# Optimization experiments

Hardware: AMD Instinct MI355X
Metric: run time of the kernel (lower is better)

The kernel has to match this reference:

```python
import jax, jax.numpy as jnp
import numpy as np

B, N, D, K = 8, 2048, 512, 16  # batch, points, feature dim, similar_num
EPS = 1e-8


def setup_inputs() -> dict:
    key = jax.random.key(0)
    ks = jax.random.split(key, 9)
    p = jax.random.normal(ks[0], (B, N, 3), dtype=jnp.float32)
    q = jax.random.normal(ks[1], (B, N, 3), dtype=jnp.float32)
    ffp = jax.random.normal(ks[2], (B, N, D), dtype=jnp.float32)
    ffq = jax.random.normal(ks[3], (B, N, D), dtype=jnp.float32)
    eye = jnp.eye(3, dtype=jnp.float32)
    # near-identity perturbed rotations so inverse is well-conditioned
    R1 = eye + 0.1 * jax.random.normal(ks[4], (B, N, 3, 3), dtype=jnp.float32)
    R2 = eye + 0.1 * jax.random.normal(ks[5], (B, N, 3, 3), dtype=jnp.float32)
    centroids = jax.random.randint(ks[6], (B, N), 0, 2 * N)  # FPS indices into 2N pts
    W = 0.02 * jax.random.normal(ks[7], (3, 3 * D), dtype=jnp.float32)  # refine_net pointwise linear
    b = jnp.zeros((3,), dtype=jnp.float32)
    return {"p": p, "q": q, "ffp": ffp, "ffq": ffq, "R1": R1, "R2": R2,
            "centroids": centroids, "W": W, "b": b}


def _forward(p, q, ffp, ffq, R1, R2, centroids, W, b):
    # cosine similarity between query features (ffq) and source features (ffp): [B,N,N]
    fq = ffq / (jnp.linalg.norm(ffq, axis=-1, keepdims=True) + EPS)
    fp = ffp / (jnp.linalg.norm(ffp, axis=-1, keepdims=True) + EPS)
    w1 = jnp.einsum('bqd,bpd->bqp', fq, fp)
    _, idx = jax.lax.top_k(w1, K)                      # [B,N,K] neighbor indices into ffp
    feat = jax.vmap(lambda z, i: z[i])(ffp, idx)       # batched gather -> [B,N,K,D]
    # adaptive_{avg,max}_pool2d over the K axis, then cat(avg, max): [B,N,2D]
    f_agg = jnp.concatenate([feat.mean(axis=2), feat.max(axis=2)], axis=-1)
    f1 = jnp.concatenate([ffq, f_agg], axis=-1)        # [B,N,3D]
    vec = jnp.einsum('bnd,od->bno', f1, W) + b         # refine_net -> [B,N,3]
    vec = jnp.linalg.inv(R1) @ vec[..., None]          # rotate back (R1^-1)
    vec = (jnp.linalg.inv(R2) @ vec)[..., 0]           # rotate back (R2^-1) -> [B,N,3]
    mask = (centroids >= p.shape[1]).astype(vec.dtype)[..., None]
    q_refine = q + vec * mask
    return q_refine, idx


def reference(p, q, ffp, ffq, R1, R2, centroids, W, b):
    q_refine, similar_idx = _forward(p, q, ffp, ffq, R1, R2, centroids, W, b)
    # original returns (q_cat, q_refine, q_refine, similar_idx)
    return (q, q_refine, q_refine, similar_idx)
```

## Files before the change

kernel.cpp:

```cpp
#include <hip/hip_runtime.h>
#include <math.h>

#define BB 8
#define NN 2048
#define DD 512
#define KK 16
#define BN (BB*NN)

#define QT 64
#define JSPLIT 4
#define JRANGE (NN/JSPLIT)
#define MM (16*JSPLIT)
#define SIMP 68

#define KSPLIT 384

#define OUT1 (BN*3)
#define OUT2 (2*BN*3)
#define OUT3 (3*BN*3)

typedef __attribute__((ext_vector_type(8))) short bf16x8;
typedef __attribute__((ext_vector_type(4))) float f32x4;

__device__ inline unsigned short cvt_bf16(float f) {
    unsigned int u = __float_as_uint(f);
    return (unsigned short)((u + 0x7fffu + ((u >> 16) & 1u)) >> 16);
}

__device__ inline void gload_lds16(const unsigned short* g, unsigned short* lds) {
    __builtin_amdgcn_global_load_lds((const __attribute__((address_space(1))) void*)g,
                                     (__attribute__((address_space(3))) void*)lds,
                                     16, 0, 0);
}

__global__ __launch_bounds__(256) void k_norm_np(const float* __restrict__ ffq,
                                                 const float* __restrict__ ffp,
                                                 float* __restrict__ normq,
                                                 float* __restrict__ normp,
                                                 float* __restrict__ rnp32) {
    const int row = blockIdx.x * 32 + (threadIdx.x >> 3);
    const int j   = threadIdx.x & 7;
    const bool isQ = row < BN;
    const int r = isQ ? row : row - BN;
    const float* x = (isQ ? ffq : ffp) + (size_t)r * DD;

    float B[4];
#pragma unroll
    for (int t = 0; t < 4; ++t) {
        const float* xb = x + t * 128;
        float e = xb[j];
        float rj = __fmul_rn(e, e);
#pragma unroll
        for (int i = 1; i < 16; ++i) {
            float v = xb[8 * i + j];
            rj = __fadd_rn(rj, __fmul_rn(v, v));
        }
        float s = __fadd_rn(rj, __shfl_xor(rj, 1, 8));
        float u = __fadd_rn(s,  __shfl_xor(s,  2, 8));
        float w = __fadd_rn(u,  __shfl_xor(u,  4, 8));
        B[t] = w;
    }
    if (j == 0) {
        float norm2 = __fadd_rn(__fadd_rn(B[0], B[1]), __fadd_rn(B[2], B[3]));
        float nrm = __fsqrt_rn(norm2);
        if (isQ) { normq[r] = nrm; }
        else {
            normp[r] = nrm;
            rnp32[r] = 1.0f / __fadd_rn(nrm, 1e-8f);
        }
    }
}

__global__ __launch_bounds__(256) void k_normalize(const float* __restrict__ ffq,
                                                   const float* __restrict__ ffp,
                                                   const float* __restrict__ normq,
                                                   const float* __restrict__ normp,
                                                   float* __restrict__ fqn,
                                                   float* __restrict__ fpn,
                                                   unsigned short* __restrict__ fqb,
                                                   unsigned short* __restrict__ fpb) {
    const size_t e4 = ((size_t)blockIdx.x * 256 + threadIdx.x) * 4;
    if (e4 >= (size_t)BN * DD) return;
    const int row = (int)(e4 >> 9);
    {
        float4 v = *(const float4*)(ffq + e4);
        float den = __fadd_rn(normq[row], 1e-8f);
        float4 o;
        o.x = __fdiv_rn(v.x, den); o.y = __fdiv_rn(v.y, den);
        o.z = __fdiv_rn(v.z, den); o.w = __fdiv_rn(v.w, den);
        *(float4*)(fqn + e4) = o;
        ushort4 b; b.x = cvt_bf16(o.x); b.y = cvt_bf16(o.y);
        b.z = cvt_bf16(o.z); b.w = cvt_bf16(o.w);
        *(ushort4*)(fqb + e4) = b;
    }
    {
        float4 v = *(const float4*)(ffp + e4);
        float den = __fadd_rn(normp[row], 1e-8f);
        float4 o;
        o.x = __fdiv_rn(v.x, den); o.y = __fdiv_rn(v.y, den);
        o.z = __fdiv_rn(v.z, den); o.w = __fdiv_rn(v.w, den);
        *(float4*)(fpn + e4) = o;
        ushort4 b; b.x = cvt_bf16(o.x); b.y = cvt_bf16(o.y);
        b.z = cvt_bf16(o.z); b.w = cvt_bf16(o.w);
        *(ushort4*)(fpb + e4) = b;
    }
}

#define CK 128
__global__ __launch_bounds__(256, 4) void k_phase1_m(const unsigned short* __restrict__ fqb,
                                                     const unsigned short* __restrict__ fpb,
                                                     unsigned short* __restrict__ cand) {
    __shared__ __align__(16) float simb[QT * SIMP];
    __shared__ __align__(16) unsigned short Bst[64 * CK];

    const int b  = blockIdx.x & 7;
    const int i0 = ((blockIdx.x >> 3) & 31) * QT;
    const int js = blockIdx.x >> 8;
    const int tid = threadIdx.x;
    const int w = tid >> 6, lane = tid & 63;
    const int n16 = lane & 15, quad = lane >> 4;

    const unsigned short* Aq = fqb + ((size_t)b * NN + i0 + w * 16 + n16) * DD + quad * 8;

    float tv[16]; int tix[16];
#pragma unroll
    for (int r = 0; r < 16; ++r) { tv[r] = -INFINITY; tix[r] = -1; }

    const int qq = tid >> 2;
    const int st = tid & 3;
    const size_t bNN = (size_t)b * NN;

    for (int jt = 0; jt < JRANGE / 64; ++jt) {
        const int j0g = js * JRANGE + jt * 64;

        f32x4 acc[4];
#pragma unroll
        for (int ct = 0; ct < 4; ++ct) acc[ct] = (f32x4){0.f, 0.f, 0.f, 0.f};

        for (int kc = 0; kc < 4; ++kc) {
            __syncthreads();
#pragma unroll
            for (int l = 0; l < 4; ++l) {
                const int r  = (w * 4 + l) * 4 + quad;
                const int sb = n16 ^ (r & 15);
                const unsigned short* gsrc =
                    fpb + (bNN + j0g + r) * DD + kc * CK + sb * 8;
                gload_lds16(gsrc, &Bst[(w * 4 + l) * 512]);
            }
            int koff = kc * 128;
            asm volatile("" : "+v"(koff));
            bf16x8 a0 = *(const bf16x8*)(Aq + koff);
            bf16x8 a1 = *(const bf16x8*)(Aq + koff + 32);
            bf16x8 a2 = *(const bf16x8*)(Aq + koff + 64);
            bf16x8 a3 = *(const bf16x8*)(Aq + koff + 96);
            __syncthreads();
#pragma unroll
            for (int k4 = 0; k4 < 4; ++k4) {
                const bf16x8 af = (k4 == 0) ? a0 : (k4 == 1) ? a1 : (k4 == 2) ? a2 : a3;
#pragma unroll
                for (int ct = 0; ct < 4; ++ct) {
                    const int r  = ct * 16 + n16;
                    const int cb = (k4 * 4 + quad) ^ (r & 15);
                    bf16x8 bfr = *(const bf16x8*)&Bst[r * CK + cb * 8];
                    acc[ct] = __builtin_amdgcn_mfma_f32_16x16x32_bf16(
                        af, bfr, acc[ct], 0, 0, 0);
                }
            }
        }

        __syncthreads();
#pragma unroll
        for (int ct = 0; ct < 4; ++ct)
#pragma unroll
            for (int r = 0; r < 4; ++r)
                simb[(w * 16 + quad * 4 + r) * SIMP + ct * 16 + n16] = acc[ct][r];
        __syncthreads();

#pragma unroll
        for (int t4 = 0; t4 < 4; ++t4) {
            const float4 v4 = *(const float4*)&simb[qq * SIMP + st * 16 + t4 * 4];
            const float vm = fmaxf(fmaxf(v4.x, v4.y), fmaxf(v4.z, v4.w));
            if (vm > tv[0]) {
                const float vv[4] = {v4.x, v4.y, v4.z, v4.w};
#pragma unroll
                for (int u = 0; u < 4; ++u) {
                    const float v = vv[u];
                    const int jg = j0g + st * 16 + t4 * 4 + u;
                    if (v > tv[0]) {
#pragma unroll
                        for (int r = 0; r < 15; ++r) {
                            const bool up = tv[r + 1] < v;
                            const float nv = up ? tv[r + 1] : ((tv[r] < v) ? v : tv[r]);
                            const int   ni = up ? tix[r + 1] : ((tv[r] < v) ? jg : tix[r]);
                            tv[r] = nv; tix[r] = ni;
                        }
                        if (tv[15] < v) { tv[15] = v; tix[15] = jg; }
                    }
                }
            }
        }
    }

    __syncthreads();
    int p = 15;
    const size_t base = ((size_t)b * NN + i0 + qq) * MM + (size_t)js * 16;
    for (int m = 0; m < 16; ++m) {
        float cv = (p >= 0) ? tv[p] : -INFINITY;
        int   ci = (p >= 0) ? tix[p] : -1;
        float ov; int oi;
        ov = __shfl_xor(cv, 1, 4); oi = __shfl_xor(ci, 1, 4);
        if (ov > cv || (ov == cv && (unsigned)oi < (unsigned)ci)) { cv = ov; ci = oi; }
        ov = __shfl_xor(cv, 2, 4); oi = __shfl_xor(ci, 2, 4);
        if (ov > cv || (ov == cv && (unsigned)oi < (unsigned)ci)) { cv = ov; ci = oi; }
        if (p >= 0 && tv[p] == cv && tix[p] == ci) --p;
        if (st == 0) cand[base + m] = (unsigned short)ci;
    }
}

#define JTILE 64
#define BK 16
#define LDP 68
__global__ __launch_bounds__(256, 4) void k_phase1_v(const float* __restrict__ ffq,
                                                     const float* __restrict__ ffp,
                                                     const float* __restrict__ rnp32,
                                                     unsigned short* __restrict__ cand) {
    __shared__ __align__(16) float As[BK * LDP];
    __shared__ __align__(16) float Bs[BK * LDP];
    __shared__ __align__(16) float simb[QT * SIMP];

    const int b  = blockIdx.x & 7;
    const int i0 = ((blockIdx.x >> 3) & 31) * QT;
    const int js = blockIdx.x >> 8;
    const int tid = threadIdx.x;
    const int tx = tid & 15, ty = tid >> 4;

    const float* Abase = ffq + ((size_t)b * NN + i0) * DD;
    const float* Bbase = ffp + (size_t)b * NN * DD;

    float tv[16]; int tix[16];
#pragma unroll
    for (int r = 0; r < 16; ++r) { tv[r] = -INFINITY; tix[r] = -1; }

    const int lrow = tid >> 2;
    const int lseg = (tid & 3) * 4;
    const int qq = tid >> 2;
    const int st = tid & 3;

    for (int jt = 0; jt < JRANGE / JTILE; ++jt) {
        const int j0 = js * JRANGE + jt * JTILE;
        float acc[4][4];
#pragma unroll
        for (int r = 0; r < 4; ++r)
#pragma unroll
            for (int c = 0; c < 4; ++c) acc[r][c] = 0.0f;

        for (int kt = 0; kt < DD / BK; ++kt) {
            const int k0 = kt * BK;
            __syncthreads();
            float4 av = *(const float4*)(Abase + (size_t)lrow * DD + k0 + lseg);
            float4 bv = *(const float4*)(Bbase + (size_t)(j0 + lrow) * DD + k0 + lseg);
            As[(lseg + 0) * LDP + lrow] = av.x; As[(lseg + 1) * LDP + lrow] = av.y;
            As[(lseg + 2) * LDP + lrow] = av.z; As[(lseg + 3) * LDP + lrow] = av.w;
            Bs[(lseg + 0) * LDP + lrow] = bv.x; Bs[(lseg + 1) * LDP + lrow] = bv.y;
            Bs[(lseg + 2) * LDP + lrow] = bv.z; Bs[(lseg + 3) * LDP + lrow] = bv.w;
            __syncthreads();
#pragma unroll
            for (int kk = 0; kk < BK; ++kk) {
                const float4 a4 = *(const float4*)&As[kk * LDP + ty * 4];
                const float4 b4 = *(const float4*)&Bs[kk * LDP + tx * 4];
                const float ar[4] = {a4.x, a4.y, a4.z, a4.w};
                const float br[4] = {b4.x, b4.y, b4.z, b4.w};
#pragma unroll
                for (int r = 0; r < 4; ++r)
#pragma unroll
                    for (int c = 0; c < 4; ++c)
                        acc[r][c] = fmaf(ar[r], br[c], acc[r][c]);
            }
        }
        float rp[4];
#pragma unroll
        for (int c = 0; c < 4; ++c) rp[c] = rnp32[b * NN + j0 + tx * 4 + c];
#pragma unroll
        for (int r = 0; r < 4; ++r) {
            float4 v4;
            v4.x = acc[r][0] * rp[0]; v4.y = acc[r][1] * rp[1];
            v4.z = acc[r][2] * rp[2]; v4.w = acc[r][3] * rp[3];
            *(float4*)&simb[(ty * 4 + r) * SIMP + tx * 4] = v4;
        }
        __syncthreads();

#pragma unroll
        for (int t = 0; t < 16; ++t) {
            const int jl = st * 16 + t;
            const float v = simb[qq * SIMP + jl];
            const int jg = j0 + jl;
            if (v > tv[0]) {
#pragma unroll
                for (int r = 0; r < 15; ++r) {
                    const bool up = tv[r + 1] < v;
                    const float nv = up ? tv[r + 1] : ((tv[r] < v) ? v : tv[r]);
                    const int   ni = up ? tix[r + 1] : ((tv[r] < v) ? jg : tix[r]);
                    tv[r] = nv; tix[r] = ni;
                }
                if (tv[15] < v) { tv[15] = v; tix[15] = jg; }
            }
        }
        __syncthreads();
    }

    int p = 15;
    const size_t base = ((size_t)b * NN + i0 + qq) * MM + (size_t)js * 16;
    for (int m = 0; m < 16; ++m) {
        float cv = (p >= 0) ? tv[p] : -INFINITY;
        int   ci = (p >= 0) ? tix[p] : -1;
        float ov; int oi;
        ov = __shfl_xor(cv, 1, 4); oi = __shfl_xor(ci, 1, 4);
        if (ov > cv || (ov == cv && (unsigned)oi < (unsigned)ci)) { cv = ov; ci = oi; }
        ov = __shfl_xor(cv, 2, 4); oi = __shfl_xor(ci, 2, 4);
        if (ov > cv || (ov == cv && (unsigned)oi < (unsigned)ci)) { cv = ov; ci = oi; }
        if (p >= 0 && tv[p] == cv && tix[p] == ci) --p;
        if (st == 0) cand[base + m] = (unsigned short)ci;
    }
}

__device__ inline void inv3_apply(const double* a, double x0, double x1, double x2,
                                  double& y0, double& y1, double& y2) {
    double c00 = a[4]*a[8] - a[5]*a[7];
    double c01 = a[2]*a[7] - a[1]*a[8];
    double c02 = a[1]*a[5] - a[2]*a[4];
    double c10 = a[5]*a[6] - a[3]*a[8];
    double c11 = a[0]*a[8] - a[2]*a[6];
    double c12 = a[2]*a[3] - a[0]*a[5];
    double c20 = a[3]*a[7] - a[4]*a[6];
    double c21 = a[1]*a[6] - a[0]*a[7];
    double c22 = a[0]*a[4] - a[1]*a[3];
    double det = a[0]*c00 + a[1]*c10 + a[2]*c20;
    double id = 1.0 / det;
    y0 = (c00*x0 + c01*x1 + c02*x2) * id;
    y1 = (c10*x0 + c11*x1 + c12*x2) * id;
    y2 = (c20*x0 + c21*x1 + c22*x2) * id;
}

#define STG_S 67
template <bool PRE>
__device__ inline void phase2_body(
        const float* __restrict__ qin, const float* __restrict__ ffq,
        const float* __restrict__ ffp, const float* __restrict__ R1,
        const float* __restrict__ R2, const int* __restrict__ cent,
        const float* __restrict__ W, const float* __restrict__ bvec,
        const float* __restrict__ normq, const float* __restrict__ normp,
        const float* __restrict__ fqn, const float* __restrict__ fpn,
        const unsigned short* __restrict__ cand, float* __restrict__ out) {
    static_assert(KSPLIT == 384, "chunk split at c=6 assumes KSPLIT==384");
    static_assert(MM * STG_S >= 2 * DD, "meanf/maxf overlay needs 2*DD floats");
    const int b = blockIdx.x & 7;
    const int i = blockIdx.x >> 3;
    const int tid = threadIdx.x;
    const size_t qi = (size_t)b * NN + i;

    __shared__ float sfqn[DD];
    __shared__ int cj[MM];
    __shared__ float pden_s[MM];
    __shared__ float sv[MM];
    __shared__ int sel[KK];
    __shared__ __align__(16) float stg[MM * STG_S];
    __shared__ float red[3][4];
    float* const meanf = stg;
    float* const maxf  = stg + DD;

    if (PRE) {
        for (int d = tid; d < DD; d += 256)
            sfqn[d] = fqn[qi * DD + d];
    } else {
        const float qden = __fadd_rn(normq[qi], 1e-8f);
        for (int d = tid; d < DD; d += 256)
            sfqn[d] = __fdiv_rn(ffq[qi * DD + d], qden);
    }
    if (tid < MM) {
        int j = (int)cand[qi * MM + tid];
        cj[tid] = j;
        if (!PRE) pden_s[tid] = __fadd_rn(normp[(size_t)b * NN + j], 1e-8f);
    }
    __syncthreads();

    const int srow = tid >> 2;
    const int slan = tid & 3;
    const float* fprow = (PRE ? fpn : ffp) + ((size_t)b * NN + cj[srow]) * DD;
    const float pd = (!PRE) ? pden_s[tid < MM ? tid : 0] : 1.0f;
    float acc1 = 0.0f, acc2 = 0.0f;

    auto stg_write = [&](const float4* P) {
#pragma unroll
        for (int i4 = 0; i4 < 4; ++i4) {
            const int off = srow * STG_S + i4 * 16 + slan * 4;
            stg[off + 0] = P[i4].x; stg[off + 1] = P[i4].y;
            stg[off + 2] = P[i4].z; stg[off + 3] = P[i4].w;
        }
    };
    auto ld_chunk = [&](float4* P, int c) {
#pragma unroll
        for (int i4 = 0; i4 < 4; ++i4)
            P[i4] = *(const float4*)(fprow + c * 64 + i4 * 16 + slan * 4);
    };
    auto chain = [&](int c, float& acc) {
        const int d0 = c * 64;
        const float* s = stg + tid * STG_S;
        if (PRE) {
#pragma unroll
            for (int k = 0; k < 64; ++k)
                acc = fmaf(sfqn[d0 + k], s[k], acc);
        } else {
#pragma unroll
            for (int k = 0; k < 64; ++k)
                acc = fmaf(sfqn[d0 + k], __fdiv_rn(s[k], pd), acc);
        }
    };

    float4 pA[4], pB[4];
    ld_chunk(pA, 0);
#pragma unroll
    for (int ch = 0; ch < 4; ++ch) {
        {
            const int c0 = 2 * ch;
            stg_write(pA);
            ld_chunk(pB, c0 + 1);
            __syncthreads();
            if (tid < MM) chain(c0, (c0 < 6) ? acc1 : acc2);
            __syncthreads();
        }
        {
            const int c1 = 2 * ch + 1;
            stg_write(pB);
            if (ch < 3) ld_chunk(pA, c1 + 1);
            __syncthreads();
            if (tid < MM) chain(c1, (c1 < 6) ? acc1 : acc2);
            __syncthreads();
        }
    }
    if (tid < MM) sv[tid] = __fadd_rn(acc1, acc2);
    __syncthreads();

    if (tid < MM) {
        const float v = sv[tid]; const int jj = cj[tid];
        int rank = 0;
        for (int t = 0; t < MM; ++t) {
            const float vt = sv[t]; const int jo = cj[t];
            rank += (vt > v) || (vt == v && jo < jj);
        }
        if (rank < KK) {
            sel[rank] = jj;
            out[(size_t)OUT3 + qi * KK + rank] = (float)jj;
        }
    }
    __syncthreads();

    for (int d = tid; d < DD; d += 256) {
        float sum = 0.0f, mx = -INFINITY;
#pragma unroll
        for (int k = 0; k < KK; ++k) {
            float v = ffp[((size_t)b * NN + sel[k]) * DD + d];
            sum += v; mx = fmaxf(mx, v);
        }
        meanf[d] = sum * (1.0f / 16.0f);
        maxf[d]  = mx;
    }
    __syncthreads();

    float a0 = 0.f, a1 = 0.f, a2 = 0.f;
    for (int d = tid; d < DD; d += 256) {
        const float x = ffq[qi * DD + d], m = meanf[d], mx = maxf[d];
        a0 = fmaf(W[d],        x, a0); a0 = fmaf(W[512 + d],        m, a0); a0 = fmaf(W[1024 + d],        mx, a0);
        a1 = fmaf(W[1536 + d], x, a1); a1 = fmaf(W[1536 + 512 + d], m, a1); a1 = fmaf(W[1536 + 1024 + d], mx, a1);
        a2 = fmaf(W[3072 + d], x, a2); a2 = fmaf(W[3072 + 512 + d], m, a2); a2 = fmaf(W[3072 + 1024 + d], mx, a2);
    }
#pragma unroll
    for (int off = 32; off > 0; off >>= 1) {
        a0 += __shfl_down(a0, off, 64);
        a1 += __shfl_down(a1, off, 64);
        a2 += __shfl_down(a2, off, 64);
    }
    const int lane = tid & 63, wid = tid >> 6;
    if (lane == 0) { red[0][wid] = a0; red[1][wid] = a1; red[2][wid] = a2; }
    __syncthreads();

    if (tid == 0) {
        double v0 = (double)bvec[0] + red[0][0] + red[0][1] + red[0][2] + red[0][3];
        double v1 = (double)bvec[1] + red[1][0] + red[1][1] + red[1][2] + red[1][3];
        double v2 = (double)bvec[2] + red[2][0] + red[2][1] + red[2][2] + red[2][3];
        double r1[9], r2[9];
#pragma unroll
        for (int t = 0; t < 9; ++t) { r1[t] = R1[qi * 9 + t]; r2[t] = R2[qi * 9 + t]; }
        double u0, u1, u2, w0, w1, w2;
        inv3_apply(r1, v0, v1, v2, u0, u1, u2);
        inv3_apply(r2, u0, u1, u2, w0, w1, w2);
        const float mask = (cent[qi] >= NN) ? 1.0f : 0.0f;
        const float q0 = qin[qi * 3 + 0], q1 = qin[qi * 3 + 1], q2 = qin[qi * 3 + 2];
        out[qi * 3 + 0] = q0; out[qi * 3 + 1] = q1; out[qi * 3 + 2] = q2;
        const float o0 = q0 + (float)w0 * mask;
        const float o1 = q1 + (float)w1 * mask;
        const float o2 = q2 + (float)w2 * mask;
        out[OUT1 + qi * 3 + 0] = o0; out[OUT1 + qi * 3 + 1] = o1; out[OUT1 + qi * 3 + 2] = o2;
        out[OUT2 + qi * 3 + 0] = o0; out[OUT2 + qi * 3 + 1] = o1; out[OUT2 + qi * 3 + 2] = o2;
    }
}

__global__ __launch_bounds__(256, 8) void k_phase2_f(
        const float* qin, const float* ffq, const float* ffp, const float* R1,
        const float* R2, const int* cent, const float* W, const float* bvec,
        const float* fqn, const float* fpn, const unsigned short* cand, float* out) {
    phase2_body<true>(qin, ffq, ffp, R1, R2, cent, W, bvec,
                      nullptr, nullptr, fqn, fpn, cand, out);
}

__global__ __launch_bounds__(256, 8) void k_phase2_v(
        const float* qin, const float* ffq, const float* ffp, const float* R1,
        const float* R2, const int* cent, const float* W, const float* bvec,
        const float* normq, const float* normp, const unsigned short* cand, float* out) {
    phase2_body<false>(qin, ffq, ffp, R1, R2, cent, W, bvec,
                       normq, normp, nullptr, nullptr, cand, out);
}

extern "C" void kernel_launch(void* const* d_in, const int* in_sizes, int n_in,
                              void* d_out, int out_size, void* d_ws, size_t ws_size,
                              hipStream_t stream) {
    (void)in_sizes; (void)n_in; (void)out_size;
    const float* q   = (const float*)d_in[1];
    const float* ffp = (const float*)d_in[2];
    const float* ffq = (const float*)d_in[3];
    const float* R1  = (const float*)d_in[4];
    const float* R2  = (const float*)d_in[5];
    const int*   ct  = (const int*)d_in[6];
    const float* W   = (const float*)d_in[7];
    const float* bb  = (const float*)d_in[8];
    float* out = (float*)d_out;

    float* normq = (float*)d_ws;
    float* normp = normq + BN;
    float* rnp32 = normp + BN;
    unsigned short* cand = (unsigned short*)(rnp32 + BN);
    float* fqn = (float*)(cand + (size_t)BN * MM);
    float* fpn = fqn + (size_t)BN * DD;
    unsigned short* fqb = (unsigned short*)(fpn + (size_t)BN * DD);
    unsigned short* fpb = fqb + (size_t)BN * DD;

    const size_t need = (size_t)BN * (35 * 4 + 2 * DD * 4 + 2 * DD * 2);

    k_norm_np<<<dim3((2 * BN) / 32), dim3(256), 0, stream>>>(ffq, ffp, normq, normp, rnp32);

    if (ws_size >= need) {
        k_normalize<<<dim3((BN * DD) / 1024), dim3(256), 0, stream>>>(
            ffq, ffp, normq, normp, fqn, fpn, fqb, fpb);
        k_phase1_m<<<dim3(BB * (NN / QT) * JSPLIT), dim3(256), 0, stream>>>(fqb, fpb, cand);
        k_phase2_f<<<dim3(BB * NN), dim3(256), 0, stream>>>(q, ffq, ffp, R1, R2, ct, W, bb,
                                                            fqn, fpn, cand, out);
    } else {
        k_phase1_v<<<dim3(BB * (NN / QT) * JSPLIT), dim3(256), 0, stream>>>(ffq, ffp, rnp32, cand);
        k_phase2_v<<<dim3(BB * NN), dim3(256), 0, stream>>>(q, ffq, ffp, R1, R2, ct, W, bb,
                                                            normq, normp, cand, out);
    }
}
```

Baseline: 461.5 us.

## Replace branchy insertion top-k with packed-key bitonic sort and merge

The per-thread top-16 tracking in the MFMA phase-1 kernel now packs each similarity and index into a 64-bit order-preserving key. Each tile's 16 candidates go through a branch-free bitonic sort, followed by a bitonic merge with the running top-16. This removes the divergent data-dependent insertion loop and lets the final cross-lane reduction compare single keys. In exchange every tile always pays the full sort-and-merge cost, which the old threshold check could skip, and 64-bit compares and selects raise register pressure.

```diff
diff --git a/kernel.cpp b/kernel.cpp
--- a/kernel.cpp
+++ b/kernel.cpp
@@ -122,9 +122,9 @@
 
     const unsigned short* Aq = fqb + ((size_t)b * NN + i0 + w * 16 + n16) * DD + quad * 8;
 
-    float tv[16]; int tix[16];
-#pragma unroll
-    for (int r = 0; r < 16; ++r) { tv[r] = -INFINITY; tix[r] = -1; }
+    unsigned long long ktop[16];
+#pragma unroll
+    for (int r = 0; r < 16; ++r) ktop[r] = 0ull;
 
     const int qq = tid >> 2;
     const int st = tid & 3;
@@ -176,44 +176,72 @@
                 simb[(w * 16 + quad * 4 + r) * SIMP + ct * 16 + n16] = acc[ct][r];
         __syncthreads();
 
+        unsigned long long nk[16];
 #pragma unroll
         for (int t4 = 0; t4 < 4; ++t4) {
             const float4 v4 = *(const float4*)&simb[qq * SIMP + st * 16 + t4 * 4];
-            const float vm = fmaxf(fmaxf(v4.x, v4.y), fmaxf(v4.z, v4.w));
-            if (vm > tv[0]) {
-                const float vv[4] = {v4.x, v4.y, v4.z, v4.w};
-#pragma unroll
-                for (int u = 0; u < 4; ++u) {
-                    const float v = vv[u];
-                    const int jg = j0g + st * 16 + t4 * 4 + u;
-                    if (v > tv[0]) {
-#pragma unroll
-                        for (int r = 0; r < 15; ++r) {
-                            const bool up = tv[r + 1] < v;
-                            const float nv = up ? tv[r + 1] : ((tv[r] < v) ? v : tv[r]);
-                            const int   ni = up ? tix[r + 1] : ((tv[r] < v) ? jg : tix[r]);
-                            tv[r] = nv; tix[r] = ni;
-                        }
-                        if (tv[15] < v) { tv[15] = v; tix[15] = jg; }
+            const float vv[4] = {v4.x, v4.y, v4.z, v4.w};
+#pragma unroll
+            for (int u = 0; u < 4; ++u) {
+                const float cvf = __fadd_rn(vv[u], 0.0f);
+                const unsigned int ub  = __float_as_uint(cvf);
+                const unsigned int ord = ub ^ (((unsigned int)((int)ub >> 31)) | 0x80000000u);
+                const unsigned int jg  = (unsigned int)(j0g + st * 16 + t4 * 4 + u);
+                nk[t4 * 4 + u] = ((unsigned long long)ord << 32)
+                               | (unsigned long long)(~jg);
+            }
+        }
+#pragma unroll
+        for (int k = 2; k <= 16; k <<= 1) {
+#pragma unroll
+            for (int j = k >> 1; j > 0; j >>= 1) {
+#pragma unroll
+                for (int i = 0; i < 16; ++i) {
+                    const int l = i ^ j;
+                    if (l > i) {
+                        const bool up = ((i & k) == 0);
+                        const unsigned long long a = nk[i], bq = nk[l];
+                        const bool sw = up ? (a > bq) : (a < bq);
+                        nk[i] = sw ? bq : a;
+                        nk[l] = sw ? a : bq;
                     }
                 }
             }
         }
+        unsigned long long mg[16];
+#pragma unroll
+        for (int i = 0; i < 16; ++i) {
+            const unsigned long long a = ktop[i], bq = nk[15 - i];
+            mg[i] = (a > bq) ? a : bq;
+        }
+#pragma unroll
+        for (int j = 8; j > 0; j >>= 1) {
+#pragma unroll
+            for (int i = 0; i < 16; ++i) {
+                const int l = i ^ j;
+                if (l > i) {
+                    const unsigned long long a = mg[i], bq = mg[l];
+                    const bool sw = a > bq;
+                    mg[i] = sw ? bq : a;
+                    mg[l] = sw ? a : bq;
+                }
+            }
+        }
+#pragma unroll
+        for (int i = 0; i < 16; ++i) ktop[i] = mg[i];
     }
 
     __syncthreads();
     int p = 15;
     const size_t base = ((size_t)b * NN + i0 + qq) * MM + (size_t)js * 16;
     for (int m = 0; m < 16; ++m) {
-        float cv = (p >= 0) ? tv[p] : -INFINITY;
-        int   ci = (p >= 0) ? tix[p] : -1;
-        float ov; int oi;
-        ov = __shfl_xor(cv, 1, 4); oi = __shfl_xor(ci, 1, 4);
-        if (ov > cv || (ov == cv && (unsigned)oi < (unsigned)ci)) { cv = ov; ci = oi; }
-        ov = __shfl_xor(cv, 2, 4); oi = __shfl_xor(ci, 2, 4);
-        if (ov > cv || (ov == cv && (unsigned)oi < (unsigned)ci)) { cv = ov; ci = oi; }
-        if (p >= 0 && tv[p] == cv && tix[p] == ci) --p;
-        if (st == 0) cand[base + m] = (unsigned short)ci;
+        const unsigned long long myk = (p >= 0) ? ktop[p] : 0ull;
+        unsigned long long wk = myk;
+        unsigned long long ok;
+        ok = __shfl_xor(wk, 1, 4); if (ok > wk) wk = ok;
+        ok = __shfl_xor(wk, 2, 4); if (ok > wk) wk = ok;
+        if (p >= 0 && myk == wk) --p;
+        if (st == 0) cand[base + m] = (unsigned short)(~(unsigned int)wk);
     }
 }
 
```

Result: faster. 426.4 us (-7.6%).
